# Performance work log

Measured on AMD Instinct MI355X. Metric: run time of the kernel, lower is better.

Reference implementation:

```python
import jax, jax.numpy as jnp
import numpy as np

B, S, E, H = 4, 2048, 1024, 16
HD = E // H  # 64 head dim


def setup_inputs() -> dict:
    key = jax.random.key(0)
    ks = jax.random.split(key, 6)
    x = jax.random.normal(ks[0], (B, S, E), dtype=jnp.float32)
    mask = jax.random.randint(ks[1], (B, S, S), 0, 2, dtype=jnp.int32)
    # per-head qkv Linear(E -> 3*HD), stacked over heads: weight [H, 3*HD, E]
    lim = 1.0 / np.sqrt(E)
    Wqkv = jax.random.uniform(ks[2], (H, 3 * HD, E), minval=-lim, maxval=lim, dtype=jnp.float32)
    bqkv = jax.random.uniform(ks[3], (H, 3 * HD), minval=-lim, maxval=lim, dtype=jnp.float32)
    Wo = jax.random.uniform(ks[4], (E, E), minval=-lim, maxval=lim, dtype=jnp.float32)
    bo = jax.random.uniform(ks[5], (E,), minval=-lim, maxval=lim, dtype=jnp.float32)
    return {"x": x, "mask": mask, "Wqkv": Wqkv, "bqkv": bqkv, "Wo": Wo, "bo": bo}


def reference(x, mask, Wqkv, bqkv, Wo, bo):
    # fused per-head qkv projection: [B,S,E] x [H,3HD,E] -> [B,H,S,3HD]
    qkv = jnp.einsum('bse,hfe->bhsf', x, Wqkv) + bqkv[None, :, None, :]
    q, k, v = jnp.split(qkv, 3, axis=-1)  # each [B,H,S,HD]
    scale = 1.0 / jnp.sqrt(jnp.float32(HD))
    scores = jnp.einsum('bhqd,bhkd->bhqk', q, k) * scale  # [B,H,S,S]
    # NOTE: original masked_fill sets masked scores to 0.0 (not -inf)
    scores = jnp.where(mask[:, None, :, :] == 1, 0.0, scores)
    attn = jax.nn.softmax(scores, axis=-1)
    ctx = jnp.einsum('bhqk,bhkd->bhqd', attn, v)  # [B,H,S,HD]
    ctx = ctx.transpose(0, 2, 1, 3).reshape(B, S, E)  # concat heads
    return ctx @ Wo.T + bo
```

## Files before the change

### kernel.cpp

```cpp
#include <hip/hip_runtime.h>
#include <stdint.h>

#define B_ 4
#define S_ 2048
#define E_ 1024
#define H_ 16
#define HD_ 64

typedef __attribute__((ext_vector_type(8))) short bf16x8;
typedef __attribute__((ext_vector_type(4))) float f32x4;

__device__ __forceinline__ ushort f2b(float f) {
    union { float f; uint32_t u; } c; c.f = f;
    return (ushort)((c.u + 0x8000u) >> 16);
}

__device__ __forceinline__ uint32_t pkbf(float a, float b) {
    union { float f; uint32_t u; } ca, cb; ca.f = a; cb.f = b;
#if __has_builtin(__builtin_amdgcn_perm)
    return __builtin_amdgcn_perm(cb.u + 0x8000u, ca.u + 0x8000u, 0x07060302u);
#else
    return (uint32_t)f2b(a) | ((uint32_t)f2b(b) << 16);
#endif
}

#if __has_builtin(__builtin_amdgcn_exp2f)
#define EXP2(x) __builtin_amdgcn_exp2f(x)
#else
#define EXP2(x) exp2f(x)
#endif

__device__ __forceinline__ void gl2lds16(const ushort* g, const ushort* l) {
    __builtin_amdgcn_global_load_lds(
        (const __attribute__((address_space(1))) unsigned int*)g,
        (__attribute__((address_space(3))) unsigned int*)l,
        16, 0, 0);
}

__global__ __launch_bounds__(256) void cvt_all(
    const float* __restrict__ x, const float* __restrict__ wq, const float* __restrict__ wo,
    ushort* __restrict__ xb, ushort* __restrict__ wqb, ushort* __restrict__ wob) {
    int i = blockIdx.x * 256 + threadIdx.x;
    const float* src; ushort* dst; int off;
    if (i < 2097152)      { src = x;  dst = xb;  off = i; }
    else if (i < 2883584) { src = wq; dst = wqb; off = i - 2097152; }
    else                  { src = wo; dst = wob; off = i - 2883584; }
    float4 f = ((const float4*)src)[off];
    ushort4 o;
    o.x = f2b(f.x); o.y = f2b(f.y); o.z = f2b(f.z); o.w = f2b(f.w);
    ((ushort4*)dst)[off] = o;
}

__global__ __launch_bounds__(256) void pack_mask(const int* __restrict__ mask,
                                                 uint32_t* __restrict__ mb) {
    int i = blockIdx.x * 256 + threadIdx.x;
    unsigned long long bal = __ballot(mask[i] == 1);
    int lane = threadIdx.x & 63;
    if (lane < 2) {
        int b = i >> 22, q = (i >> 11) & 2047, c = i & 2047;
        int kt = c >> 6;
        mb[((uint64_t)(b * 32 + kt) * 2048 + q) * 2 + lane] =
            (lane == 0) ? (uint32_t)bal : (uint32_t)(bal >> 32);
    }
}

template <int KD>
__device__ __forceinline__ void gemm_bt_core(
    const ushort* __restrict__ A, const ushort* __restrict__ Bm,
    int m0, int n0, ushort* L, f32x4 (&acc)[4][4])
{
    constexpr int NST = KD / 32;
    const int tid  = threadIdx.x;
    const int lane = tid & 63;
    const int wave = tid >> 6;
    const int wm = wave >> 1, wn = wave & 1;
    const int fr = lane & 15;
    const int fk = (lane >> 4) * 8;
    const int lrow = lane >> 2;
    const int lk   = (lane & 3) * 8;

    const f32x4 fz = {0.f, 0.f, 0.f, 0.f};
#pragma unroll
    for (int i = 0; i < 4; ++i)
#pragma unroll
        for (int j = 0; j < 4; ++j) acc[i][j] = fz;

    ushort* s0 = L;
    ushort* s1 = L + 8192;
    ushort* s2 = L + 16384;

    const uint64_t arow = (uint64_t)(m0 + lrow) * KD + lk;
    const uint64_t brow = (uint64_t)(n0 + lrow) * KD + lk;

#define GEMM_STAGE(k0, slot)                                                     \
    {                                                                            \
        _Pragma("unroll")                                                        \
        for (int t = 0; t < 2; ++t) {                                            \
            const int r0 = t * 64 + wave * 16;                                   \
            gl2lds16(&A [arow + (uint64_t)r0 * KD + (k0)], &(slot)[r0 * 32]);    \
            gl2lds16(&Bm[brow + (uint64_t)r0 * KD + (k0)], &(slot)[4096 + r0 * 32]); \
        }                                                                        \
    }

    GEMM_STAGE(0, s0);
    GEMM_STAGE(32, s1);
    asm volatile("s_waitcnt vmcnt(4)" ::: "memory");
    __builtin_amdgcn_s_barrier();
    __builtin_amdgcn_sched_barrier(0);

    ushort* cur = s0; ushort* nxt = s1; ushort* tgt = s2;

    for (int kt = 0; kt < NST; ++kt) {
        if (kt < NST - 2) GEMM_STAGE((kt + 2) * 32, tgt);

        bf16x8 af[4], bfr[4];
#pragma unroll
        for (int i = 0; i < 4; ++i)
            af[i] = *(const bf16x8*)&cur[(wm * 64 + i * 16 + fr) * 32 + fk];
#pragma unroll
        for (int j = 0; j < 4; ++j)
            bfr[j] = *(const bf16x8*)&cur[4096 + (wn * 64 + j * 16 + fr) * 32 + fk];
        __builtin_amdgcn_s_setprio(1);
#pragma unroll
        for (int i = 0; i < 4; ++i)
#pragma unroll
            for (int j = 0; j < 4; ++j)
                acc[i][j] = __builtin_amdgcn_mfma_f32_16x16x32_bf16(af[i], bfr[j], acc[i][j], 0, 0, 0);
        __builtin_amdgcn_s_setprio(0);

        if (kt < NST - 2) {
            asm volatile("s_waitcnt vmcnt(4)" ::: "memory");
        } else {
            asm volatile("s_waitcnt vmcnt(0)" ::: "memory");
        }
        __builtin_amdgcn_s_barrier();
        __builtin_amdgcn_sched_barrier(0);

        ushort* o = cur; cur = nxt; nxt = tgt; tgt = o;
    }
#undef GEMM_STAGE
}

__global__ __launch_bounds__(256) void qkv_gemm(
    const ushort* __restrict__ xb, const ushort* __restrict__ wb,
    const float* __restrict__ bqkv,
    ushort* __restrict__ qo, ushort* __restrict__ ko, ushort* __restrict__ vto)
{
    __shared__ __align__(16) ushort L[24576];
    f32x4 acc[4][4];
    const int lin = blockIdx.x;
    const int swz = (lin & 7) * 192 + (lin >> 3);
    const int m0 = (swz & 63) * 128;
    const int n0 = (swz >> 6) * 128;
    gemm_bt_core<1024>(xb, wb, m0, n0, L, acc);

    const int lane = threadIdx.x & 63, wave = threadIdx.x >> 6;
    const int wm = wave >> 1, wn = wave & 1;
    const int col = lane & 15, rg = lane >> 4;
    const float QSC = 0.125f * 1.4426950408889634f;
#pragma unroll
    for (int j = 0; j < 4; ++j) {
        const int n = n0 + wn * 64 + j * 16 + col;
        const int h = n / 192, f = n % 192;
        const float bias = bqkv[n];
#pragma unroll
        for (int i2 = 0; i2 < 4; ++i2) {
            const int mbase = m0 + wm * 64 + i2 * 16 + rg * 4;
            if (f < 128) {
#pragma unroll
                for (int v = 0; v < 4; ++v) {
                    const int m = mbase + v;
                    const int b = m >> 11, s = m & 2047;
                    const float val = acc[i2][j][v] + bias;
                    if (f < 64) qo[((uint64_t)(b * 16 + h) * 2048 + s) * 64 + f]        = f2b(val * QSC);
                    else        ko[((uint64_t)(b * 16 + h) * 2048 + s) * 64 + (f - 64)] = f2b(val);
                }
            } else {
                const int b = mbase >> 11, s = mbase & 2047;
                ushort4 pk;
                pk.x = f2b(acc[i2][j][0] + bias);
                pk.y = f2b(acc[i2][j][1] + bias);
                pk.z = f2b(acc[i2][j][2] + bias);
                pk.w = f2b(acc[i2][j][3] + bias);
                *(ushort4*)&vto[((uint64_t)(b * 16 + h) * 64 + (f - 128)) * 2048 + s] = pk;
            }
        }
    }
}

__global__ __launch_bounds__(256, 3) void attn_kernel(
    const ushort* __restrict__ qa, const ushort* __restrict__ ka,
    const ushort* __restrict__ vta, const uint32_t* __restrict__ mbits,
    ushort* __restrict__ ctxo)
{
    __shared__ __align__(16) ushort LDSH[24576];
    ushort* const Ks0 = LDSH;
    ushort* const Vt0 = LDSH + 4096;
    ushort* const Ks1 = LDSH + 8192;
    ushort* const Vt1 = LDSH + 12288;
    ushort* const Ks2 = LDSH + 16384;
    ushort* const Vt2 = LDSH + 20480;
    ushort* const CTX = LDSH;

    const int bid = blockIdx.x;
    const int bh = (bid & 7) * 8 + (bid >> 7);
    const int qb = (bid >> 3) & 15;
    const int b = bh >> 4;
    const int tid = threadIdx.x, lane = tid & 63, wave = tid >> 6;
    const int col = lane & 15, rg = lane >> 4;

    const uint64_t bhoff = (uint64_t)bh * (S_ * 64);
    const ushort* qp = qa + bhoff + (uint64_t)qb * 128 * 64;
    const ushort* kp = ka + bhoff;
    const ushort* vp = vta + bhoff;
    const uint32_t* mk0 = mbits + ((uint64_t)(b * 32) * 2048 + qb * 128 + wave * 32 + col) * 2;
    const uint32_t* mk1 = mk0 + 32;

    const int lr = lane >> 3;
    const int usw = (lane & 7) ^ lr;
    const int r0s = wave * 16 + lr;
    const int r1s = r0s + 8;
    const int sg0 = (r0s & 32) | ((r0s & 12) << 1) | ((r0s & 16) >> 2) | (r0s & 3);
    const int sg1 = (r1s & 32) | ((r1s & 12) << 1) | ((r1s & 16) >> 2) | (r1s & 3);
    const int kb0 = sg0 * 64 + usw * 8;
    const int kb1 = sg1 * 64 + usw * 8;
    const int vb0 = r0s * 2048 + usw * 8;
    const int vb1 = r1s * 2048 + usw * 8;
    const int ldst0 = wave * 1024;
    const int ldst1 = ldst0 + 512;

    bf16x8 aq[2][2];
#pragma unroll
    for (int i = 0; i < 2; ++i)
#pragma unroll
        for (int k2 = 0; k2 < 2; ++k2)
            aq[i][k2] = *(const bf16x8*)&qp[(wave * 32 + i * 16 + col) * 64 + k2 * 32 + rg * 8];

    gl2lds16(&kp[kb0], &Ks0[ldst0]);
    gl2lds16(&kp[kb1], &Ks0[ldst1]);
    gl2lds16(&vp[vb0], &Vt0[ldst0]);
    gl2lds16(&vp[vb1], &Vt0[ldst1]);
    uint2 m_cur0 = *(const uint2*)mk0;
    uint2 m_cur1 = *(const uint2*)mk1;
    gl2lds16(&kp[4096 + kb0], &Ks1[ldst0]);
    gl2lds16(&kp[4096 + kb1], &Ks1[ldst1]);
    gl2lds16(&vp[vb0 + 64], &Vt1[ldst0]);
    gl2lds16(&vp[vb1 + 64], &Vt1[ldst1]);
    uint2 m_nxt0 = *(const uint2*)(mk0 + 4096);
    uint2 m_nxt1 = *(const uint2*)(mk1 + 4096);
    uint2 m_new0 = m_nxt0, m_new1 = m_nxt1;
    asm volatile("s_waitcnt vmcnt(0)" ::: "memory");
    __builtin_amdgcn_s_barrier();
    __builtin_amdgcn_sched_barrier(0);

    const f32x4 fz = {0.f, 0.f, 0.f, 0.f};
    f32x4 acc[4][2];
#pragma unroll
    for (int dt = 0; dt < 4; ++dt)
#pragma unroll
        for (int i = 0; i < 2; ++i) acc[dt][i] = fz;
    f32x4 acc5[2] = {fz, fz};

    bf16x8 vone;
#pragma unroll
    for (int e = 0; e < 8; ++e) vone[e] = (short)0x3F80;

    uint32_t bsel[2][4];
#pragma unroll
    for (int p = 0; p < 2; ++p)
#pragma unroll
        for (int v = 0; v < 4; ++v) bsel[p][v] = 1u << (rg * 8 + p * 4 + v);

    const int u0 = (rg ^ (col & 7)) << 3;

    const ushort* cK = Ks0; const ushort* cV = Vt0;
    const ushort* nK = Ks1; const ushort* nV = Vt1;
    ushort* tK = Ks2; ushort* tV = Vt2;

    for (int kt = 0; kt < 32; ++kt) {
        if (kt < 30) {
            const int k2 = (kt + 2) * 4096;
            gl2lds16(&kp[k2 + kb0], &tK[ldst0]);
            gl2lds16(&kp[k2 + kb1], &tK[ldst1]);
            gl2lds16(&vp[vb0 + (kt + 2) * 64], &tV[ldst0]);
            gl2lds16(&vp[vb1 + (kt + 2) * 64], &tV[ldst1]);
            m_new0 = *(const uint2*)(mk0 + (uint64_t)(kt + 2) * 4096);
            m_new1 = *(const uint2*)(mk1 + (uint64_t)(kt + 2) * 4096);
        }

        f32x4 sc[2][4];
        __builtin_amdgcn_s_setprio(1);
#pragma unroll
        for (int j = 0; j < 4; ++j) {
            bf16x8 bk0 = *(const bf16x8*)&cK[(j * 16 + col) * 64 + u0];
            bf16x8 bk1 = *(const bf16x8*)&cK[(j * 16 + col) * 64 + (u0 ^ 32)];
#pragma unroll
            for (int i = 0; i < 2; ++i) {
                f32x4 z = __builtin_amdgcn_mfma_f32_16x16x32_bf16(bk0, aq[i][0], fz, 0, 0, 0);
                sc[i][j] = __builtin_amdgcn_mfma_f32_16x16x32_bf16(bk1, aq[i][1], z, 0, 0, 0);
            }
        }
        __builtin_amdgcn_s_setprio(0);

        bf16x8 bp[2][2];
#pragma unroll
        for (int i = 0; i < 2; ++i) {
            const uint2 mw = i ? m_cur1 : m_cur0;
            union { uint32_t w[4]; bf16x8 v; } p0, p1;
#pragma unroll
            for (int j = 0; j < 4; ++j) {
                const uint32_t w = (j & 2) ? mw.y : mw.x;
                const int p = j & 1;
                float pe[4];
#pragma unroll
                for (int v = 0; v < 4; ++v) {
                    const float s = (w & bsel[p][v]) ? 0.f : sc[i][j][v];
                    pe[v] = EXP2(s);
                }
                const uint32_t lo = pkbf(pe[0], pe[1]);
                const uint32_t hi = pkbf(pe[2], pe[3]);
                if (j < 2) { p0.w[p * 2] = lo; p0.w[p * 2 + 1] = hi; }
                else       { p1.w[p * 2] = lo; p1.w[p * 2 + 1] = hi; }
            }
            bp[i][0] = p0.v;
            bp[i][1] = p1.v;
        }

        __builtin_amdgcn_s_setprio(1);
#pragma unroll
        for (int i = 0; i < 2; ++i) {
            acc5[i] = __builtin_amdgcn_mfma_f32_16x16x32_bf16(vone, bp[i][0], acc5[i], 0, 0, 0);
            acc5[i] = __builtin_amdgcn_mfma_f32_16x16x32_bf16(vone, bp[i][1], acc5[i], 0, 0, 0);
        }
#pragma unroll
        for (int dt = 0; dt < 4; ++dt) {
            bf16x8 av0 = *(const bf16x8*)&cV[(dt * 16 + col) * 64 + u0];
            bf16x8 av1 = *(const bf16x8*)&cV[(dt * 16 + col) * 64 + (u0 ^ 32)];
#pragma unroll
            for (int i = 0; i < 2; ++i) {
                acc[dt][i] = __builtin_amdgcn_mfma_f32_16x16x32_bf16(av0, bp[i][0], acc[dt][i], 0, 0, 0);
                acc[dt][i] = __builtin_amdgcn_mfma_f32_16x16x32_bf16(av1, bp[i][1], acc[dt][i], 0, 0, 0);
            }
        }
        __builtin_amdgcn_s_setprio(0);

        if (kt < 30) {
            asm volatile("s_waitcnt vmcnt(6)" ::: "memory");
        } else {
            asm volatile("s_waitcnt vmcnt(0)" ::: "memory");
        }
        __builtin_amdgcn_s_barrier();
        __builtin_amdgcn_sched_barrier(0);

        const ushort* oK = cK; const ushort* oV = cV;
        cK = nK; cV = nV; nK = tK; nV = tV; tK = (ushort*)oK; tV = (ushort*)oV;
        m_cur0 = m_nxt0; m_cur1 = m_nxt1; m_nxt0 = m_new0; m_nxt1 = m_new1;
    }

    float linv[2];
#pragma unroll
    for (int i = 0; i < 2; ++i) linv[i] = 1.0f / acc5[i][0];

#pragma unroll
    for (int dt = 0; dt < 4; ++dt)
#pragma unroll
        for (int i = 0; i < 2; ++i) {
            const int q = wave * 32 + i * 16 + col;
            const int d = dt * 16 + rg * 4;
            const int gg = (d >> 3) ^ (q & 7);
            ushort4 pk;
            pk.x = f2b(acc[dt][i][0] * linv[i]);
            pk.y = f2b(acc[dt][i][1] * linv[i]);
            pk.z = f2b(acc[dt][i][2] * linv[i]);
            pk.w = f2b(acc[dt][i][3] * linv[i]);
            *(ushort4*)&CTX[q * 64 + gg * 8 + (d & 7)] = pk;
        }
    __syncthreads();
    const int h = bh & 15;
    const uint64_t obase = (uint64_t)(b * S_ + qb * 128) * E_ + (uint64_t)h * 64;
#pragma unroll
    for (int t4 = 0; t4 < 4; ++t4) {
        const int id = tid + t4 * 256;
        const int r = id >> 3, c8 = id & 7;
        *(bf16x8*)&ctxo[obase + (uint64_t)r * E_ + c8 * 8] =
            *(const bf16x8*)&CTX[r * 64 + ((c8 ^ (r & 7)) << 3)];
    }
}

__global__ __launch_bounds__(256) void out_gemm(
    const ushort* __restrict__ ctxb, const ushort* __restrict__ wob,
    const float* __restrict__ bo, float* __restrict__ out)
{
    __shared__ __align__(16) ushort L[24576];
    f32x4 acc[4][4];
    const int lin = blockIdx.x;
    const int swz = (lin & 7) * 64 + (lin >> 3);
    const int m0 = (swz & 63) * 128;
    const int n0 = (swz >> 6) * 128;
    gemm_bt_core<1024>(ctxb, wob, m0, n0, L, acc);

    const int lane = threadIdx.x & 63, wave = threadIdx.x >> 6;
    const int wm = wave >> 1, wn = wave & 1;
    const int col = lane & 15, rg = lane >> 4;
#pragma unroll
    for (int j = 0; j < 4; ++j) {
        const int n = n0 + wn * 64 + j * 16 + col;
        const float bias = bo[n];
#pragma unroll
        for (int i2 = 0; i2 < 4; ++i2) {
            const int mb2 = m0 + wm * 64 + i2 * 16 + rg * 4;
#pragma unroll
            for (int v = 0; v < 4; ++v)
                out[(uint64_t)(mb2 + v) * 1024 + n] = acc[i2][j][v] + bias;
        }
    }
}

extern "C" void kernel_launch(void* const* d_in, const int* in_sizes, int n_in,
                              void* d_out, int out_size, void* d_ws, size_t ws_size,
                              hipStream_t stream)
{
    const float* x    = (const float*)d_in[0];
    const int*   mask = (const int*)d_in[1];
    const float* Wqkv = (const float*)d_in[2];
    const float* bqkv = (const float*)d_in[3];
    const float* Wo   = (const float*)d_in[4];
    const float* bo   = (const float*)d_in[5];
    float* out = (float*)d_out;

    char* p = (char*)d_ws;
    ushort* xb  = (ushort*)p; p += (size_t)8388608 * 2;
    ushort* wqb = (ushort*)p; p += (size_t)3145728 * 2;
    ushort* wob = (ushort*)p; p += (size_t)1048576 * 2;
    ushort* qo  = (ushort*)p; p += (size_t)8388608 * 2;
    ushort* ko  = (ushort*)p; p += (size_t)8388608 * 2;
    ushort* vto = (ushort*)p; p += (size_t)8388608 * 2;
    ushort* ctx = (ushort*)p; p += (size_t)8388608 * 2;
    uint32_t* mb = (uint32_t*)p;

    cvt_all<<<12288, 256, 0, stream>>>(x, Wqkv, Wo, xb, wqb, wob);
    pack_mask<<<65536, 256, 0, stream>>>(mask, mb);
    qkv_gemm<<<1536, 256, 0, stream>>>(xb, wqb, bqkv, qo, ko, vto);
    attn_kernel<<<1024, 256, 0, stream>>>(qo, ko, vto, mb, ctx);
    out_gemm<<<512, 256, 0, stream>>>(ctx, wob, bo, out);
}
```

Measured before the change: 359.3 us.

## Shrink V tile buffering to double-buffer to fit four blocks per CU

The attention kernel keeps K triple-buffered but moves V to double buffering, prefetching V one tile ahead instead of two. That cuts LDS per block from 48KB to 40KB, and the launch-bounds hint is raised from 3 to 4 blocks per CU to match. Wait counts are adjusted to the new number of outstanding loads. The shorter V prefetch distance may expose more load latency, and four blocks per CU constrains registers further.

```diff
diff --git a/kernel.cpp b/kernel.cpp
--- a/kernel.cpp
+++ b/kernel.cpp
@@ -188,18 +188,17 @@
     }
 }
 
-__global__ __launch_bounds__(256, 3) void attn_kernel(
+__global__ __launch_bounds__(256, 4) void attn_kernel(
     const ushort* __restrict__ qa, const ushort* __restrict__ ka,
     const ushort* __restrict__ vta, const uint32_t* __restrict__ mbits,
     ushort* __restrict__ ctxo)
 {
-    __shared__ __align__(16) ushort LDSH[24576];
-    ushort* const Ks0 = LDSH;
-    ushort* const Vt0 = LDSH + 4096;
-    ushort* const Ks1 = LDSH + 8192;
-    ushort* const Vt1 = LDSH + 12288;
-    ushort* const Ks2 = LDSH + 16384;
-    ushort* const Vt2 = LDSH + 20480;
+    __shared__ __align__(16) ushort LDSH[20480];
+    ushort* const Ka0 = LDSH;
+    ushort* const Ka1 = LDSH + 4096;
+    ushort* const Ka2 = LDSH + 8192;
+    ushort* const Va0 = LDSH + 12288;
+    ushort* const Va1 = LDSH + 16384;
     ushort* const CTX = LDSH;
 
     const int bid = blockIdx.x;
@@ -236,16 +235,14 @@
         for (int k2 = 0; k2 < 2; ++k2)
             aq[i][k2] = *(const bf16x8*)&qp[(wave * 32 + i * 16 + col) * 64 + k2 * 32 + rg * 8];
 
-    gl2lds16(&kp[kb0], &Ks0[ldst0]);
-    gl2lds16(&kp[kb1], &Ks0[ldst1]);
-    gl2lds16(&vp[vb0], &Vt0[ldst0]);
-    gl2lds16(&vp[vb1], &Vt0[ldst1]);
+    gl2lds16(&kp[kb0], &Ka0[ldst0]);
+    gl2lds16(&kp[kb1], &Ka0[ldst1]);
+    gl2lds16(&vp[vb0], &Va0[ldst0]);
+    gl2lds16(&vp[vb1], &Va0[ldst1]);
+    gl2lds16(&kp[4096 + kb0], &Ka1[ldst0]);
+    gl2lds16(&kp[4096 + kb1], &Ka1[ldst1]);
     uint2 m_cur0 = *(const uint2*)mk0;
     uint2 m_cur1 = *(const uint2*)mk1;
-    gl2lds16(&kp[4096 + kb0], &Ks1[ldst0]);
-    gl2lds16(&kp[4096 + kb1], &Ks1[ldst1]);
-    gl2lds16(&vp[vb0 + 64], &Vt1[ldst0]);
-    gl2lds16(&vp[vb1 + 64], &Vt1[ldst1]);
     uint2 m_nxt0 = *(const uint2*)(mk0 + 4096);
     uint2 m_nxt1 = *(const uint2*)(mk1 + 4096);
     uint2 m_new0 = m_nxt0, m_new1 = m_nxt1;
@@ -273,17 +270,19 @@
 
     const int u0 = (rg ^ (col & 7)) << 3;
 
-    const ushort* cK = Ks0; const ushort* cV = Vt0;
-    const ushort* nK = Ks1; const ushort* nV = Vt1;
-    ushort* tK = Ks2; ushort* tV = Vt2;
+    const ushort* cK = Ka0; const ushort* nK = Ka1; ushort* tK = Ka2;
+    const ushort* cV = Va0; ushort* nV = Va1;
 
     for (int kt = 0; kt < 32; ++kt) {
+        if (kt < 31) {
+            gl2lds16(&vp[vb0 + (kt + 1) * 64], &nV[ldst0]);
+            gl2lds16(&vp[vb1 + (kt + 1) * 64], &nV[ldst1]);
+        }
+        __builtin_amdgcn_sched_barrier(0);
         if (kt < 30) {
             const int k2 = (kt + 2) * 4096;
             gl2lds16(&kp[k2 + kb0], &tK[ldst0]);
             gl2lds16(&kp[k2 + kb1], &tK[ldst1]);
-            gl2lds16(&vp[vb0 + (kt + 2) * 64], &tV[ldst0]);
-            gl2lds16(&vp[vb1 + (kt + 2) * 64], &tV[ldst1]);
             m_new0 = *(const uint2*)(mk0 + (uint64_t)(kt + 2) * 4096);
             m_new1 = *(const uint2*)(mk1 + (uint64_t)(kt + 2) * 4096);
         }
@@ -345,15 +344,16 @@
         __builtin_amdgcn_s_setprio(0);
 
         if (kt < 30) {
-            asm volatile("s_waitcnt vmcnt(6)" ::: "memory");
+            asm volatile("s_waitcnt vmcnt(4)" ::: "memory");
         } else {
             asm volatile("s_waitcnt vmcnt(0)" ::: "memory");
         }
         __builtin_amdgcn_s_barrier();
         __builtin_amdgcn_sched_barrier(0);
 
-        const ushort* oK = cK; const ushort* oV = cV;
-        cK = nK; cV = nV; nK = tK; nV = tV; tK = (ushort*)oK; tV = (ushort*)oV;
+        const ushort* oK = cK;
+        cK = nK; nK = tK; tK = (ushort*)oK;
+        ushort* oV = (ushort*)cV; cV = nV; nV = oV;
         m_cur0 = m_nxt0; m_cur1 = m_nxt1; m_nxt0 = m_new0; m_nxt1 = m_new1;
     }
 
```

Measured after the change: 374.4 us. +4.2%, slower.
